# Optimization experiments

Measured on AMD Instinct MI355X. Metric: run time of the kernel, lower is better.

The kernel has to match this reference:

```python
import jax, jax.numpy as jnp
import numpy as np

N_HEAD = 16

def setup_inputs() -> dict:
    key = jax.random.key(0)
    ks = jax.random.split(key, 5)
    B, T, C = 2, 2048, 1024
    s = 1.0 / np.sqrt(C)
    return {
        "x":  jax.random.normal(ks[0], (B, T, C), jnp.float32),
        "Wk": jax.random.normal(ks[1], (C, C), jnp.float32) * s,
        "Wq": jax.random.normal(ks[2], (C, C), jnp.float32) * s,
        "Wv": jax.random.normal(ks[3], (C, C), jnp.float32) * s,
        "Wp": jax.random.normal(ks[4], (C, C), jnp.float32) * s,
    }

def reference(x, Wk, Wq, Wv, Wp):
    B, T, C = x.shape
    H = N_HEAD
    D = C // H
    # torch Linear (bias=False): y = x @ W.T
    def proj(W):
        return (x @ W.T).reshape(B, T, H, D).transpose(0, 2, 1, 3)  # [B,H,T,D]
    q, k, v = proj(Wq), proj(Wk), proj(Wv)
    att = jnp.einsum("bhtd,bhsd->bhts", q, k) / jnp.sqrt(jnp.float32(D))
    causal = jnp.tril(jnp.ones((T, T), dtype=bool))
    att = jnp.where(causal[None, None], att, -jnp.inf)
    att = jax.nn.softmax(att, axis=-1)
    y = jnp.einsum("bhts,bhsd->bhtd", att, v)
    y = y.transpose(0, 2, 1, 3).reshape(B, T, C)
    return y @ Wp.T
```

## Files before the change

kernel.cpp:

```cpp
#include <hip/hip_runtime.h>

typedef unsigned short u16;
typedef unsigned int u32;
typedef unsigned long long u64;
typedef __attribute__((ext_vector_type(8))) short bf16x8;
typedef __attribute__((ext_vector_type(8))) _Float16 f16x8;
typedef __attribute__((ext_vector_type(4))) float f32x4;
typedef __attribute__((ext_vector_type(4))) u32 u32x4;

#define GLOAD16(gp, lp) __builtin_amdgcn_global_load_lds( \
  (const __attribute__((address_space(1))) unsigned int*)(gp), \
  (__attribute__((address_space(3))) unsigned int*)(lp), 16, 0, 0)

__device__ __forceinline__ u16 f2bf(float f) {
  unsigned int u = __builtin_bit_cast(unsigned int, f);
  u += 0x7fffu + ((u >> 16) & 1u);
  return (u16)(u >> 16);
}

__device__ __forceinline__ u32 pk2(float a, float b) {
  return (u32)f2bf(a) | ((u32)f2bf(b) << 16);
}

__device__ __forceinline__ u32 pkh(float a, float b) {
  return __builtin_bit_cast(u32, __builtin_amdgcn_cvt_pkrtz(a, b));
}

__device__ __forceinline__ void wait_barrier() {
  asm volatile("s_waitcnt vmcnt(0)" ::: "memory");
  __builtin_amdgcn_s_barrier();
  __builtin_amdgcn_sched_barrier(0);
}

__global__ __launch_bounds__(256) void cvt_all(
    const float* __restrict__ x,
    const float* __restrict__ w0, const float* __restrict__ w1,
    const float* __restrict__ w2, const float* __restrict__ w3,
    u16* __restrict__ ox, u16* __restrict__ o0, u16* __restrict__ o1,
    u16* __restrict__ o2, u16* __restrict__ o3) {
  int bid = blockIdx.x;
  const float* in; u16* out; size_t off;
  if (bid < 4096) {
    in = x; out = ox; off = (size_t)bid << 10;
  } else {
    int r = bid - 4096, z = r >> 10;
    in  = (z == 0) ? w0 : (z == 1) ? w1 : (z == 2) ? w2 : w3;
    out = (z == 0) ? o0 : (z == 1) ? o1 : (z == 2) ? o2 : o3;
    off = (size_t)(r & 1023) << 10;
  }
  size_t i = off + (size_t)threadIdx.x * 4;
  float4 f = *reinterpret_cast<const float4*>(in + i);
  u64 v = (u64)pk2(f.x, f.y) | ((u64)pk2(f.z, f.w) << 32);
  *reinterpret_cast<u64*>(out + i) = v;
}

template<int MODE, int MT, int NT>
__device__ __forceinline__ void gemm_bt_body(
    const u16* __restrict__ A, const u16* __restrict__ Bw, void* __restrict__ Cout,
    int m0, int n0, float scale) {
  const int K = 1024;
  __shared__ __align__(16) u16 As[2][MT * 32];
  __shared__ __align__(16) u16 Bs[2][NT * 32];
  const int tid = threadIdx.x;
  const int lane = tid & 63, wid = tid >> 6;
  const int wr = wid >> 1, wc = wid & 1;
  const int g = lane >> 4, c = lane & 15;
  f32x4 acc[MT / 32][NT / 32] = {};

  auto stage = [&](int buf, int k0) {
#pragma unroll
    for (int i = 0; i < MT / 64; ++i) {
      int idx = tid + i * 256;
      int row = idx >> 2, slot = idx & 3;
      int ss = slot ^ (row & 3);
      GLOAD16(A + (size_t)(m0 + row) * K + k0 + ss * 8, &As[buf][idx * 8]);
    }
#pragma unroll
    for (int i = 0; i < NT / 64; ++i) {
      int idx = tid + i * 256;
      int row = idx >> 2, slot = idx & 3;
      int ss = slot ^ (row & 3);
      GLOAD16(Bw + (size_t)(n0 + row) * K + k0 + ss * 8, &Bs[buf][idx * 8]);
    }
  };

  stage(0, 0);
  int buf = 0;
#pragma unroll 1
  for (int kt = 0; kt < 32; ++kt) {
    wait_barrier();
    if (kt + 1 < 32) stage(buf ^ 1, (kt + 1) * 32);
    bf16x8 af[MT / 32], bfr[NT / 32];
#pragma unroll
    for (int mi = 0; mi < MT / 32; ++mi) {
      int row = wr * (MT / 2) + mi * 16 + c;
      int slot = g ^ (row & 3);
      af[mi] = *(const bf16x8*)&As[buf][row * 32 + slot * 8];
    }
#pragma unroll
    for (int ni = 0; ni < NT / 32; ++ni) {
      int row = wc * (NT / 2) + ni * 16 + c;
      int slot = g ^ (row & 3);
      bfr[ni] = *(const bf16x8*)&Bs[buf][row * 32 + slot * 8];
    }
    __builtin_amdgcn_s_setprio(1);
#pragma unroll
    for (int mi = 0; mi < MT / 32; ++mi)
#pragma unroll
      for (int ni = 0; ni < NT / 32; ++ni)
        acc[mi][ni] = __builtin_amdgcn_mfma_f32_16x16x32_bf16(af[mi], bfr[ni], acc[mi][ni], 0, 0, 0);
    __builtin_amdgcn_s_setprio(0);
    buf ^= 1;
  }

#pragma unroll
  for (int mi = 0; mi < MT / 32; ++mi)
#pragma unroll
    for (int ni = 0; ni < NT / 32; ++ni)
#pragma unroll
      for (int i = 0; i < 4; ++i) {
        int m = m0 + wr * (MT / 2) + mi * 16 + g * 4 + i;
        int n = n0 + wc * (NT / 2) + ni * 16 + c;
        float v = acc[mi][ni][i];
        if (MODE == 0) {
          int b = m >> 11, t = m & 2047, h = n >> 6, d = n & 63;
          ((u16*)Cout)[(((size_t)b * 16 + h) * 2048 + t) * 64 + d] = f2bf(v * scale);
        } else {
          ((float*)Cout)[(size_t)m * 1024 + n] = v;
        }
      }
}

#define QSCALE 0.1803368801111204f

__global__ __launch_bounds__(256, 3) void proj_qkv(
    const u16* __restrict__ xb, const u16* __restrict__ wq, const u16* __restrict__ wk,
    const u16* __restrict__ wv, u16* __restrict__ q, u16* __restrict__ k, u16* __restrict__ v) {
  int z = blockIdx.z;
  const u16* W = (z == 0) ? wq : (z == 1) ? wk : wv;
  u16* O = (z == 0) ? q : (z == 1) ? k : v;
  float scale = (z == 0) ? QSCALE : 1.0f;
  gemm_bt_body<0, 128, 128>(xb, W, O, blockIdx.y * 128, blockIdx.x * 128, scale);
}

__global__ __launch_bounds__(256, 4) void gemm_out(
    const u16* __restrict__ y, const u16* __restrict__ wp, float* __restrict__ out) {
  gemm_bt_body<1, 64, 64>(y, wp, out, blockIdx.y * 64, blockIdx.x * 64, 1.0f);
}

__global__ __launch_bounds__(256) void transpose_v_kernel(
    const u16* __restrict__ v, u16* __restrict__ vt) {
  __shared__ u16 tile[64][65];
  int bh = blockIdx.y, t0 = blockIdx.x * 64;
  const u16* src = v + ((size_t)bh * 2048 + t0) * 64;
  u16* dst = vt + (size_t)bh * 64 * 2048 + t0;
  int tid = threadIdx.x;
#pragma unroll
  for (int i = 0; i < 16; ++i) {
    int idx = tid + i * 256;
    tile[idx >> 6][idx & 63] = src[idx];
  }
  __syncthreads();
#pragma unroll
  for (int i = 0; i < 16; ++i) {
    int idx = tid + i * 256;
    int d = idx >> 6, j = idx & 63;
    int t = (((((j >> 2) & 1) << 1) | (j >> 5)) << 4) | (((j >> 3) & 3) << 2) | (j & 3);
    float f = __builtin_bit_cast(float, (u32)tile[t][d] << 16);
    _Float16 hh = (_Float16)f;
    dst[(size_t)d * 2048 + j] = __builtin_bit_cast(u16, hh);
  }
}

__global__ __launch_bounds__(256, 4) void attn_kernel(
    const u16* __restrict__ q, const u16* __restrict__ kg,
    const u16* __restrict__ vt, u16* __restrict__ y) {
  const int T = 2048;
  __shared__ __align__(16) u16 Ks[2][64 * 64];
  __shared__ __align__(16) u16 Vs[2][64 * 64];
  const int tid = threadIdx.x, lane = tid & 63, w = tid >> 6;
  const int g = lane >> 4, c = lane & 15;
  const int bh = blockIdx.x;
  const int yy = blockIdx.y, m8 = yy >> 3, o8 = yy & 7;
  const int qt = (m8 == 0) ? o8 : (m8 == 1) ? 31 - o8 : (m8 == 2) ? 8 + o8 : 23 - o8;
  const u16* Q = q + (size_t)bh * T * 64;
  const u16* K = kg + (size_t)bh * T * 64;
  const u16* V = vt + (size_t)bh * 64 * T;
  const int b = bh >> 4, h = bh & 15;
  const int qrow0 = qt * 64 + w * 16;

  f16x8 ones;
#pragma unroll
  for (int j = 0; j < 8; ++j) ones[j] = (_Float16)1.0f;

  auto stage = [&](int bb, int j0) {
#pragma unroll
    for (int i = 0; i < 2; ++i) {
      int idx = tid + i * 256;
      int row = idx >> 3, slot = idx & 7;
      int ss = slot ^ (row & 7);
      GLOAD16(K + (size_t)(j0 + row) * 64 + ss * 8, &Ks[bb][idx * 8]);
      GLOAD16(V + (size_t)row * T + j0 + ss * 8, &Vs[bb][idx * 8]);
    }
  };

  bf16x8 qf[2];
#pragma unroll
  for (int kk = 0; kk < 2; ++kk)
    qf[kk] = *(const bf16x8*)&Q[(size_t)(qrow0 + c) * 64 + kk * 32 + g * 8];

  f32x4 o[4] = {};
  f32x4 ol = {};

  const int nkt = qt + 1;
  stage(0, 0);
  int buf = 0;
#pragma unroll 1
  for (int kt = 0; kt < nkt; ++kt) {
    const int j0 = kt * 64;
    wait_barrier();
    if (kt + 1 < nkt) stage(buf ^ 1, j0 + 64);

    bf16x8 kb[4][2];
#pragma unroll
    for (int ni = 0; ni < 4; ++ni)
#pragma unroll
      for (int kk = 0; kk < 2; ++kk) {
        int kr = ni * 16 + c;
        int slot = (kk * 4 + g) ^ (kr & 7);
        kb[ni][kk] = *(const bf16x8*)&Ks[buf][kr * 64 + slot * 8];
      }
    f32x4 s[4];
    __builtin_amdgcn_s_setprio(1);
#pragma unroll
    for (int ni = 0; ni < 4; ++ni) {
      f32x4 a = {0.f, 0.f, 0.f, 0.f};
      a = __builtin_amdgcn_mfma_f32_16x16x32_bf16(kb[ni][0], qf[0], a, 0, 0, 0);
      a = __builtin_amdgcn_mfma_f32_16x16x32_bf16(kb[ni][1], qf[1], a, 0, 0, 0);
      s[ni] = a;
    }
    __builtin_amdgcn_s_setprio(0);

    const bool dumask = (kt == qt);
#pragma unroll
    for (int ni = 0; ni < 4; ++ni)
#pragma unroll
      for (int i = 0; i < 4; ++i) {
        float val = s[ni][i];
        if (dumask) {
          int key = j0 + ni * 16 + g * 4 + i;
          if (key > qrow0 + c) val = -3.0e38f;
        }
        s[ni][i] = __builtin_amdgcn_exp2f(val);
      }

    u32x4 pa0 = { pkh(s[0][0], s[0][1]), pkh(s[0][2], s[0][3]),
                  pkh(s[2][0], s[2][1]), pkh(s[2][2], s[2][3]) };
    u32x4 pa1 = { pkh(s[1][0], s[1][1]), pkh(s[1][2], s[1][3]),
                  pkh(s[3][0], s[3][1]), pkh(s[3][2], s[3][3]) };
    f16x8 pa[2];
    pa[0] = __builtin_bit_cast(f16x8, pa0);
    pa[1] = __builtin_bit_cast(f16x8, pa1);

    f16x8 vb[4][2];
#pragma unroll
    for (int di = 0; di < 4; ++di)
#pragma unroll
      for (int kk = 0; kk < 2; ++kk) {
        int d = di * 16 + c;
        int slot = (kk * 4 + g) ^ (d & 7);
        vb[di][kk] = *(const f16x8*)&Vs[buf][d * 64 + slot * 8];
      }
    __builtin_amdgcn_s_setprio(1);
    ol = __builtin_amdgcn_mfma_f32_16x16x32_f16(pa[0], ones, ol, 0, 0, 0);
    ol = __builtin_amdgcn_mfma_f32_16x16x32_f16(pa[1], ones, ol, 0, 0, 0);
#pragma unroll
    for (int di = 0; di < 4; ++di) {
      o[di] = __builtin_amdgcn_mfma_f32_16x16x32_f16(pa[0], vb[di][0], o[di], 0, 0, 0);
      o[di] = __builtin_amdgcn_mfma_f32_16x16x32_f16(pa[1], vb[di][1], o[di], 0, 0, 0);
    }
    __builtin_amdgcn_s_setprio(0);
    buf ^= 1;
  }

#pragma unroll
  for (int i = 0; i < 4; ++i) {
    float inv = 1.f / ol[i];
    int t = qrow0 + g * 4 + i;
#pragma unroll
    for (int di = 0; di < 4; ++di) {
      int col = h * 64 + di * 16 + c;
      y[((size_t)b * 2048 + t) * 1024 + col] = f2bf(o[di][i] * inv);
    }
  }
}

extern "C" void kernel_launch(void* const* d_in, const int* in_sizes, int n_in,
                              void* d_out, int out_size, void* d_ws, size_t ws_size,
                              hipStream_t stream) {
  const float* x  = (const float*)d_in[0];
  const float* Wk = (const float*)d_in[1];
  const float* Wq = (const float*)d_in[2];
  const float* Wv = (const float*)d_in[3];
  const float* Wp = (const float*)d_in[4];
  float* out = (float*)d_out;

  char* ws = (char*)d_ws;
  const size_t SZ_X = (size_t)4096 * 1024 * 2;
  const size_t SZ_W = (size_t)1024 * 1024 * 2;
  u16* xb  = (u16*)(ws);
  u16* qb  = (u16*)(ws + SZ_X);
  u16* kb  = (u16*)(ws + 2 * SZ_X);
  u16* vb  = (u16*)(ws + 3 * SZ_X);
  u16* wqb = (u16*)(ws + 4 * SZ_X);
  u16* wkb = (u16*)(ws + 4 * SZ_X + SZ_W);
  u16* wvb = (u16*)(ws + 4 * SZ_X + 2 * SZ_W);
  u16* wpb = (u16*)(ws + 4 * SZ_X + 3 * SZ_W);

  cvt_all<<<8192, 256, 0, stream>>>(x, Wq, Wk, Wv, Wp, xb, wqb, wkb, wvb, wpb);

  proj_qkv<<<dim3(8, 32, 3), 256, 0, stream>>>(xb, wqb, wkb, wvb, qb, kb, vb);

  u16* vtb = xb;
  transpose_v_kernel<<<dim3(32, 32), 256, 0, stream>>>(vb, vtb);

  u16* yb = vb;
  attn_kernel<<<dim3(32, 32), 256, 0, stream>>>(qb, kb, vtb, yb);

  gemm_out<<<dim3(16, 64), 256, 0, stream>>>(yb, wpb, out);
}
```

Baseline: 108.8 us.

## Split long causal query tiles across two blocks and combine partial results

Query tiles 16-31, which have the longest causal key ranges, now each run as two blocks that cover half the key tiles. Their unnormalized outputs and row sums go to scratch buffers (the output tensor and the Wq bf16 workspace are reused), and a new combine kernel adds the halves and normalizes. This balances per-block work and raises the block count from 1024 to 1536 to cut the long-tail imbalance. The cost is an extra kernel launch and fp32 scratch traffic. The split is correct only because the softmax path appears to use no running max, so the partial sums can simply be added.

After: 109.8 us. Within noise of the previous version (+0.9%).

```diff
diff --git a/kernel.cpp b/kernel.cpp
--- a/kernel.cpp
+++ b/kernel.cpp
@@ -174,15 +174,28 @@
 
 __global__ __launch_bounds__(256, 4) void attn_kernel(
     const u16* __restrict__ q, const u16* __restrict__ kg,
-    const u16* __restrict__ vt, u16* __restrict__ y) {
+    const u16* __restrict__ vt, u16* __restrict__ y,
+    float* __restrict__ Os, float* __restrict__ Ls) {
   const int T = 2048;
   __shared__ __align__(16) u16 Ks[2][64 * 64];
   __shared__ __align__(16) u16 Vs[2][64 * 64];
   const int tid = threadIdx.x, lane = tid & 63, w = tid >> 6;
   const int g = lane >> 4, c = lane & 15;
   const int bh = blockIdx.x;
-  const int yy = blockIdx.y, m8 = yy >> 3, o8 = yy & 7;
-  const int qt = (m8 == 0) ? o8 : (m8 == 1) ? 31 - o8 : (m8 == 2) ? 8 + o8 : 23 - o8;
+  const int yy = blockIdx.y;
+  const bool partial = (yy < 32);
+  int qt, k0t, k1t, part = 0;
+  if (partial) {
+    qt = 16 + (yy >> 1);
+    part = yy & 1;
+    int nt = qt + 1, h1 = nt >> 1;
+    k0t = part ? h1 : 0;
+    k1t = part ? nt : h1;
+  } else {
+    qt = 47 - yy;
+    k0t = 0;
+    k1t = qt + 1;
+  }
   const u16* Q = q + (size_t)bh * T * 64;
   const u16* K = kg + (size_t)bh * T * 64;
   const u16* V = vt + (size_t)bh * 64 * T;
@@ -212,14 +225,13 @@
   f32x4 o[4] = {};
   f32x4 ol = {};
 
-  const int nkt = qt + 1;
-  stage(0, 0);
+  stage(0, k0t * 64);
   int buf = 0;
 #pragma unroll 1
-  for (int kt = 0; kt < nkt; ++kt) {
+  for (int kt = k0t; kt < k1t; ++kt) {
     const int j0 = kt * 64;
     wait_barrier();
-    if (kt + 1 < nkt) stage(buf ^ 1, j0 + 64);
+    if (kt + 1 < k1t) stage(buf ^ 1, j0 + 64);
 
     bf16x8 kb[4][2];
 #pragma unroll
@@ -283,15 +295,53 @@
     buf ^= 1;
   }
 
-#pragma unroll
-  for (int i = 0; i < 4; ++i) {
-    float inv = 1.f / ol[i];
-    int t = qrow0 + g * 4 + i;
-#pragma unroll
-    for (int di = 0; di < 4; ++di) {
-      int col = h * 64 + di * 16 + c;
-      y[((size_t)b * 2048 + t) * 1024 + col] = f2bf(o[di][i] * inv);
-    }
+  if (!partial) {
+#pragma unroll
+    for (int i = 0; i < 4; ++i) {
+      float inv = 1.f / ol[i];
+      int t = qrow0 + g * 4 + i;
+#pragma unroll
+      for (int di = 0; di < 4; ++di) {
+        int col = h * 64 + di * 16 + c;
+        y[((size_t)b * 2048 + t) * 1024 + col] = f2bf(o[di][i] * inv);
+      }
+    }
+  } else {
+    int tile = (bh << 4) + (qt - 16);
+    float* Op = Os + ((size_t)(tile * 2 + part) << 12);
+#pragma unroll
+    for (int i = 0; i < 4; ++i) {
+      int row = w * 16 + g * 4 + i;
+#pragma unroll
+      for (int di = 0; di < 4; ++di)
+        Op[row * 64 + di * 16 + c] = o[di][i];
+    }
+    if (c == 0) {
+      float* Lp = Ls + ((tile * 2 + part) << 6);
+#pragma unroll
+      for (int i = 0; i < 4; ++i)
+        Lp[w * 16 + g * 4 + i] = ol[i];
+    }
+  }
+}
+
+__global__ __launch_bounds__(256) void attn_combine(
+    const float* __restrict__ Os, const float* __restrict__ Ls,
+    u16* __restrict__ y) {
+  int tile = blockIdx.x, t = threadIdx.x;
+  int bh = tile >> 4, qt = 16 + (tile & 15);
+  int b = bh >> 4, h = bh & 15;
+  const float* O0 = Os + ((size_t)tile * 2 << 12);
+  const float* O1 = O0 + 4096;
+  const float* L0 = Ls + ((size_t)tile * 2 << 6);
+  const float* L1 = L0 + 64;
+#pragma unroll
+  for (int j = 0; j < 16; ++j) {
+    int e = j * 256 + t;
+    int row = e >> 6, d = e & 63;
+    float l = L0[row] + L1[row];
+    float v = (O0[e] + O1[e]) / l;
+    y[((size_t)b * 2048 + qt * 64 + row) * 1024 + h * 64 + d] = f2bf(v);
   }
 }
 
@@ -324,8 +374,12 @@
   u16* vtb = xb;
   transpose_v_kernel<<<dim3(32, 32), 256, 0, stream>>>(vb, vtb);
 
+  float* Os = out;
+  float* Ls = (float*)wqb;
+
   u16* yb = vb;
-  attn_kernel<<<dim3(32, 32), 256, 0, stream>>>(qb, kb, vtb, yb);
+  attn_kernel<<<dim3(32, 48), 256, 0, stream>>>(qb, kb, vtb, yb, Os, Ls);
+  attn_combine<<<512, 256, 0, stream>>>(Os, Ls, yb);
 
   gemm_out<<<dim3(16, 64), 256, 0, stream>>>(yb, wpb, out);
 }
```
